# Performance work log

Measured on AMD Instinct MI355X. Metric: run time of the kernel, lower is better.

The kernel has to match this reference:

```python
import jax, jax.numpy as jnp
import numpy as np

CONF_THRESH = 0.01
TOP_K = 200
NMS_THRESH = 0.45


def setup_inputs() -> dict:
    key = jax.random.key(0)
    k1, k2, k3, k4, k5 = jax.random.split(key, 5)
    B, N, C = 32, 8732, 21
    return {
        "loc_data": jax.random.normal(k1, (B, N, 4), jnp.float32),
        "conf_data": jax.random.normal(k2, (B, N, C), jnp.float32),
        "pose_data": jax.random.normal(k3, (B, N, 32), jnp.float32),
        "line_data": jax.random.normal(k4, (B, N, 3), jnp.float32),
        "dbox_list": jax.random.uniform(k5, (N, 4), jnp.float32),
    }


def decode(loc, dbox):
    # loc, dbox: [N,4]; variances 0.1 / 0.2 as in the torch decode()
    cxcy = dbox[:, :2] + loc[:, :2] * 0.1 * dbox[:, 2:]
    wh = dbox[:, 2:] * jnp.exp(loc[:, 2:] * 0.2)
    mins = cxcy - wh / 2.0
    maxs = mins + wh
    return jnp.concatenate([mins, maxs], axis=1)  # [N,4] xyxy


def nms_class(boxes, scores, poses, lines):
    """Greedy NMS for one (batch, class). boxes [N,4], scores [N] (softmax probs).
    Matches torch nm_suppression: candidates are the top_k by score above
    conf_thresh; suppress IoU > overlap; at most top_k kept."""
    s0 = jnp.where(scores > CONF_THRESH, scores, -jnp.inf)
    _, cand_idx = jax.lax.top_k(s0, TOP_K)  # descending-score candidate pool
    cb = boxes[cand_idx]                     # [K,4]
    cs = s0[cand_idx]                        # [K], -inf where below threshold
    x1, y1, x2, y2 = cb[:, 0], cb[:, 1], cb[:, 2], cb[:, 3]
    area = (x2 - x1) * (y2 - y1)
    K = TOP_K
    ar = jnp.arange(K)

    def step(s, _):
        i = jnp.argmax(s)
        take = jnp.isfinite(s[i])
        xx1 = jnp.maximum(x1, x1[i])
        yy1 = jnp.maximum(y1, y1[i])
        xx2 = jnp.minimum(x2, x2[i])
        yy2 = jnp.minimum(y2, y2[i])
        inter = jnp.clip(xx2 - xx1, 0.0) * jnp.clip(yy2 - yy1, 0.0)
        union = area - inter + area[i]
        iou = inter / union
        supp = (iou > NMS_THRESH) | (ar == i)
        s_new = jnp.where(take & supp, -jnp.inf, s)
        return s_new, (i, take)

    _, (pos, take) = jax.lax.scan(step, cs, None, length=K)
    gi = cand_idx[pos]  # global box indices of kept detections [K]
    row = jnp.concatenate(
        [scores[gi][:, None], boxes[gi], poses[gi], lines[gi]], axis=1
    )  # [K, 1+4+32+3] = [200, 40]
    return row * take[:, None].astype(row.dtype)


def reference(loc_data, conf_data, pose_data, line_data, dbox_list):
    conf = jax.nn.softmax(conf_data, axis=-1)                       # [B,N,C]
    boxes = jax.vmap(decode, in_axes=(0, None))(loc_data, dbox_list)  # [B,N,4]
    per_cls = jax.vmap(nms_class, in_axes=(None, 1, None, None))    # over classes
    per_batch = jax.vmap(per_cls, in_axes=(0, 0, 0, 0))             # over batch
    out = per_batch(boxes, conf, pose_data, line_data)              # [B,C,200,40]
    return out.at[:, 0].set(0.0)  # class 0 (background) is skipped in torch loop
```

## Files before the change

kernel.cpp:

```cpp
#include <hip/hip_runtime.h>
#include <math.h>

#define BB 32
#define NN 8732
#define CC 21
#define TOPK 200
#define NPOSE 32
#define NLINE 3
#define NBINS 2048
#define CAP 1024
#define ROWW 40

__device__ __forceinline__ double fexp12(double x) {
  const double LOG2E = 1.4426950408889634074;
  const double LN2HI = 6.93147180369123816490e-01;
  const double LN2LO = 1.90821492927058770002e-10;
  double kd = rint(x * LOG2E);
  double r = fma(-kd, LN2HI, x);
  r = fma(-kd, LN2LO, r);
  double p = 2.08767569878680989792e-09;
  p = fma(p, r, 2.50521083854417187751e-08);
  p = fma(p, r, 2.75573192239858906526e-07);
  p = fma(p, r, 2.75573192239858925110e-06);
  p = fma(p, r, 2.48015873015873015873e-05);
  p = fma(p, r, 1.98412698412698412698e-04);
  p = fma(p, r, 1.38888888888888888889e-03);
  p = fma(p, r, 8.33333333333333333333e-03);
  p = fma(p, r, 4.16666666666666666667e-02);
  p = fma(p, r, 1.66666666666666666667e-01);
  p = fma(p, r, 0.5);
  p = fma(p, r, 1.0);
  p = fma(p, r, 1.0);
  int k = (int)kd;
  k = k < -1020 ? -1020 : (k > 1020 ? 1020 : k);
  double sc = __longlong_as_double((long long)(1023 + k) << 52);
  return p * sc;
}

__device__ __forceinline__ double fexp_t(double x, const double* __restrict__ T) {
  const double INV64 = 1.4426950408889634074 * 64.0;
  const double L64HI = 6.93147180369123816490e-01 / 64.0;
  const double L64LO = 1.90821492927058770002e-10 / 64.0;
  double kd = rint(x * INV64);
  double r = fma(-kd, L64HI, x);
  r = fma(-kd, L64LO, r);
  double p = 4.16666666666666666667e-02;
  p = fma(p, r, 1.66666666666666666667e-01);
  p = fma(p, r, 0.5);
  p = fma(p, r, 1.0);
  p = fma(p, r, 1.0);
  int ki = (int)kd;
  double t = T[ki & 63];
  int e = ki >> 6;
  e = e < -1020 ? -1020 : e;
  double sc = __longlong_as_double((long long)(1023 + e) << 52);
  return (t * p) * sc;
}

__global__ __launch_bounds__(256, 4) void score_kernel(
    const float* __restrict__ conf, float* __restrict__ scores) {
  __shared__ __align__(16) float buf[256 * CC];
  __shared__ double Texp[64];
  const int tid = threadIdx.x;
  const int i0 = blockIdx.x * 256;
  const int base = i0 * CC;
  int total = BB * NN * CC - base;
  if (total > 256 * CC) total = 256 * CC;
  {
    const float4* g4 = (const float4*)(conf + base);
    float4* b4 = (float4*)buf;
    const int n4 = total >> 2;
    for (int t = tid; t < n4; t += 256) b4[t] = g4[t];
  }
  if (tid < 64)
    Texp[tid] = fexp12((double)tid * (6.93147180369123816490e-01 / 64.0));
  __syncthreads();
  const int i = i0 + tid;
  if (i >= BB * NN) return;
  const float* p = buf + tid * CC;
  float x[CC];
#pragma unroll
  for (int c = 0; c < CC; ++c) x[c] = p[c];
  float m = x[0];
#pragma unroll
  for (int c = 1; c < CC; ++c) m = fmaxf(m, x[c]);
  float e[CC];
#pragma unroll
  for (int c = 0; c < CC; ++c) e[c] = (float)fexp_t((double)(x[c] - m), Texp);
  float r0 = e[0] + e[8], r1 = e[1] + e[9], r2 = e[2] + e[10], r3 = e[3] + e[11];
  float r4 = e[4] + e[12], r5 = e[5] + e[13], r6 = e[6] + e[14], r7 = e[7] + e[15];
  float sum = ((r0 + r1) + (r2 + r3)) + ((r4 + r5) + (r6 + r7));
  sum += e[16]; sum += e[17]; sum += e[18]; sum += e[19]; sum += e[20];
  const int b = i / NN, n = i - b * NN;
#pragma unroll
  for (int c = 0; c < CC; ++c)
    scores[((size_t)b * CC + c) * NN + n] = e[c] / sum;
}

__device__ __forceinline__ int score_bin(float s) {
  unsigned u = __float_as_uint(s);
  int bin = (int)(u >> 15) - 30720;
  return bin < 0 ? 0 : (bin > NBINS - 1 ? NBINS - 1 : bin);
}

__device__ __forceinline__ float score_full(const float* conf, int b, int c, int n) {
  const float* p = conf + ((size_t)b * NN + n) * CC;
  float mm = p[0];
  for (int c2 = 1; c2 < CC; ++c2) mm = fmaxf(mm, p[c2]);
  float e[CC];
  for (int c2 = 0; c2 < CC; ++c2) e[c2] = (float)fexp12((double)(p[c2] - mm));
  float r0 = e[0] + e[8], r1 = e[1] + e[9], r2 = e[2] + e[10], r3 = e[3] + e[11];
  float r4 = e[4] + e[12], r5 = e[5] + e[13], r6 = e[6] + e[14], r7 = e[7] + e[15];
  float sum = ((r0 + r1) + (r2 + r3)) + ((r4 + r5) + (r6 + r7));
  sum += e[16]; sum += e[17]; sum += e[18]; sum += e[19]; sum += e[20];
  return e[c] / sum;
}

__global__ __launch_bounds__(256) void nms_kernel(
    const float* __restrict__ loc, const float* __restrict__ conf,
    const float* __restrict__ pose, const float* __restrict__ line,
    const float* __restrict__ dbox, const float* __restrict__ scores,
    int mode, float* __restrict__ out) {
  const int bc = blockIdx.x;
  const int b = bc / CC, c = bc - b * CC;
  const int tid = threadIdx.x;
  const int wv = tid >> 6, lane = tid & 63;
  float* outSlab = out + (size_t)bc * (TOPK * ROWW);
  const float4 z4 = make_float4(0.f, 0.f, 0.f, 0.f);

  if (c == 0) {
    float4* o4 = (float4*)outSlab;
    for (int i = tid; i < TOPK * ROWW / 4; i += 256) o4[i] = z4;
    return;
  }

  __shared__ int hist[NBINS];
  __shared__ __align__(16) unsigned long long ckey[CAP + 16];
  __shared__ float4 cbox[TOPK];
  __shared__ float carea[TOPK];
  __shared__ float sScore[TOPK];
  __shared__ int sIdx[TOPK];
  __shared__ unsigned long long supp[TOPK * 4];
  __shared__ unsigned long long rowAnyBits[4];
  __shared__ int kept[TOPK];
  __shared__ int waveTot[4];
  __shared__ int sBT, sCnt, sKept;

  for (int i = tid; i < NBINS; i += 256) hist[i] = 0;
  if (tid == 0) { sCnt = 0; sBT = 0; }
  __syncthreads();

  const float* scoresB = scores + ((size_t)b * CC + c) * NN;

  float4 v[9];
  if (mode == 1) {
#pragma unroll
    for (int k = 0; k < 8; ++k)
      v[k] = *(const float4*)(scoresB + k * 1024 + tid * 4);
    if (tid < 135)
      v[8] = *(const float4*)(scoresB + 8192 + tid * 4);
    else
      v[8] = make_float4(-1.f, -1.f, -1.f, -1.f);
  } else {
#pragma unroll 1
    for (int k = 0; k < 9; ++k) {
      const int n0 = k * 1024 + (tid << 2);
      if (k < 8 || tid < 135) {
        v[k].x = score_full(conf, b, c, n0 + 0);
        v[k].y = score_full(conf, b, c, n0 + 1);
        v[k].z = score_full(conf, b, c, n0 + 2);
        v[k].w = score_full(conf, b, c, n0 + 3);
      } else {
        v[k] = make_float4(-1.f, -1.f, -1.f, -1.f);
      }
    }
  }

#pragma unroll
  for (int k = 0; k < 9; ++k) {
    if (v[k].x > 0.01f) atomicAdd(&hist[score_bin(v[k].x)], 1);
    if (v[k].y > 0.01f) atomicAdd(&hist[score_bin(v[k].y)], 1);
    if (v[k].z > 0.01f) atomicAdd(&hist[score_bin(v[k].z)], 1);
    if (v[k].w > 0.01f) atomicAdd(&hist[score_bin(v[k].w)], 1);
  }
  __syncthreads();

  int s8 = 0;
#pragma unroll
  for (int k = 0; k < 8; ++k) s8 += hist[tid * 8 + k];
  int cs = s8;
#pragma unroll
  for (int d = 1; d < 64; d <<= 1) {
    int t = __shfl_down(cs, d, 64);
    if (lane + d < 64) cs += t;
  }
  if (lane == 0) waveTot[wv] = cs;
  __syncthreads();
  {
    int higher = 0;
    for (int g = wv + 1; g < 4; ++g) higher += waveTot[g];
    int incl = cs + higher;
    int excl = incl - s8;
    if (excl < TOPK && incl >= TOPK) {
      int cum = excl, bt = tid * 8;
      for (int bin = tid * 8 + 7;; --bin) {
        cum += hist[bin];
        if (cum >= TOPK || bin == tid * 8) { bt = bin; break; }
      }
      sBT = bt;
    }
  }
  __syncthreads();
  const int bt = sBT;

#pragma unroll
  for (int k = 0; k < 9; ++k) {
    float sv[4] = {v[k].x, v[k].y, v[k].z, v[k].w};
#pragma unroll
    for (int j = 0; j < 4; ++j) {
      float s = sv[j];
      if (s > 0.01f && score_bin(s) >= bt) {
        int p = atomicAdd(&sCnt, 1);
        if (p < CAP) {
          unsigned n = (unsigned)(k * 1024 + (tid << 2) + j);
          ckey[p] = ((unsigned long long)__float_as_uint(s) << 32) |
                    (unsigned long long)(0xFFFFFFFFu - n);
        }
      }
    }
  }
  __syncthreads();
  const int M = sCnt < CAP ? sCnt : CAP;
  if (M == 0) {
    float4* o4 = (float4*)outSlab;
    for (int i = tid; i < TOPK * ROWW / 4; i += 256) o4[i] = z4;
    return;
  }
  const int K = M < TOPK ? M : TOPK;
  const int Mpad = (M + 15) & ~15;
  for (int i = M + tid; i < Mpad; i += 256) ckey[i] = 0ull;
  __syncthreads();

  for (int t = tid; t < M; t += 256) {
    unsigned long long kt = ckey[t];
    int r = 0;
    for (int j0 = 0; j0 < Mpad; j0 += 16) {
      ulonglong2 kk[8];
#pragma unroll
      for (int q = 0; q < 8; ++q)
        kk[q] = *(const ulonglong2*)(ckey + j0 + 2 * q);
#pragma unroll
      for (int q = 0; q < 8; ++q) {
        r += (kk[q].x > kt) ? 1 : 0;
        r += (kk[q].y > kt) ? 1 : 0;
      }
    }
    if (r < TOPK) {
      sScore[r] = __uint_as_float((unsigned)(kt >> 32));
      sIdx[r] = (int)(0xFFFFFFFFu - (unsigned)(kt & 0xFFFFFFFFull));
    }
  }
  __syncthreads();

  const float* locB = loc + (size_t)b * NN * 4;
  if (tid < K) {
    int n = sIdx[tid];
    float4 l4 = *(const float4*)(locB + (size_t)n * 4);
    float4 d4 = *(const float4*)(dbox + (size_t)n * 4);
    float cx = d4.x + (l4.x * 0.1f) * d4.z;
    float cy = d4.y + (l4.y * 0.1f) * d4.w;
    float w = d4.z * (float)fexp12((double)(l4.z * 0.2f));
    float h = d4.w * (float)fexp12((double)(l4.w * 0.2f));
    float x1 = cx - w * 0.5f;
    float y1 = cy - h * 0.5f;
    float x2 = x1 + w;
    float y2 = y1 + h;
    cbox[tid] = make_float4(x1, y1, x2, y2);
    carea[tid] = (x2 - x1) * (y2 - y1);
  }
  __syncthreads();

  {
    const double TMID = (double)0.45f + 0x1p-26;
    const int l = wv * 64 + lane;
    const bool lvalid = l < K;
    float4 lb = lvalid ? cbox[l] : z4;
    float lar = lvalid ? carea[l] : 0.f;
    const int jlim = (K < wv * 64 + 63) ? K : (wv * 64 + 63);
    for (int j0 = 0; j0 < jlim; j0 += 8) {
      const int jc = (jlim - j0 < 8) ? (jlim - j0) : 8;
      float4 jb[8];
      float ja[8];
#pragma unroll
      for (int q = 0; q < 8; ++q)
        if (q < jc) { jb[q] = cbox[j0 + q]; ja[q] = carea[j0 + q]; }
      unsigned long long mres[8];
#pragma unroll
      for (int q = 0; q < 8; ++q) {
        if (q < jc) {
          float xx1 = fmaxf(lb.x, jb[q].x);
          float yy1 = fmaxf(lb.y, jb[q].y);
          float xx2 = fminf(lb.z, jb[q].z);
          float yy2 = fminf(lb.w, jb[q].w);
          float iw = fmaxf(xx2 - xx1, 0.0f);
          float ih = fmaxf(yy2 - yy1, 0.0f);
          float inter = iw * ih;
          float uni = (lar - inter) + ja[q];
          double tt = fma(-TMID, (double)uni, (double)inter);
          bool hit = lvalid & (l > (j0 + q)) & (tt > 0.0);
          mres[q] = __ballot((int)hit);
        }
      }
      if (lane == 0) {
#pragma unroll
        for (int q = 0; q < 8; ++q)
          if (q < jc) supp[(j0 + q) * 4 + wv] = mres[q];
      }
    }
    if (lane == 0)
      for (int j = jlim; j < K; ++j) supp[j * 4 + wv] = 0ull;
  }
  __syncthreads();

  {
    bool nz = false;
    if (tid < K)
      nz = (supp[tid * 4 + 0] | supp[tid * 4 + 1] |
            supp[tid * 4 + 2] | supp[tid * 4 + 3]) != 0ull;
    unsigned long long bal = __ballot((int)nz);
    if (lane == 0) rowAnyBits[wv] = bal;
  }
  __syncthreads();

  if (tid == 0) {
    unsigned long long alive[4];
#pragma unroll
    for (int w = 0; w < 4; ++w) {
      int cnt = K - w * 64;
      alive[w] = cnt <= 0 ? 0ull : (cnt >= 64 ? ~0ull : ((1ull << cnt) - 1ull));
    }
    int nk = 0;
#pragma unroll
    for (int w = 0; w < 4; ++w) {
      const unsigned long long raw = rowAnyBits[w];
      while (alive[w]) {
        int bit = __ffsll(alive[w]) - 1;
        int j = w * 64 + bit;
        kept[nk++] = j;
        alive[w] &= ~(1ull << bit);
        if ((raw >> bit) & 1) {
          unsigned long long r0 = supp[j * 4 + 0];
          unsigned long long r1 = supp[j * 4 + 1];
          unsigned long long r2 = supp[j * 4 + 2];
          unsigned long long r3 = supp[j * 4 + 3];
          alive[0] &= ~r0; alive[1] &= ~r1; alive[2] &= ~r2; alive[3] &= ~r3;
        }
      }
    }
    sKept = nk;
  }
  __syncthreads();

  const int nk = sKept;
  const float* poseB = pose + (size_t)b * NN * NPOSE;
  const float* lineB = line + (size_t)b * NN * NLINE;
  for (int t = tid; t < nk; t += 256) {
    int j = kept[t];
    int n = sIdx[j];
    float* row = outSlab + (size_t)t * ROWW;
    float4 bx = cbox[j];
    row[0] = sScore[j];
    row[1] = bx.x;
    row[2] = bx.y;
    row[3] = bx.z;
    row[4] = bx.w;
    const float4* p4 = (const float4*)(poseB + (size_t)n * NPOSE);
#pragma unroll
    for (int q = 0; q < 8; ++q) {
      float4 pv = p4[q];
      row[5 + 4 * q + 0] = pv.x;
      row[5 + 4 * q + 1] = pv.y;
      row[5 + 4 * q + 2] = pv.z;
      row[5 + 4 * q + 3] = pv.w;
    }
    row[37] = lineB[(size_t)n * NLINE + 0];
    row[38] = lineB[(size_t)n * NLINE + 1];
    row[39] = lineB[(size_t)n * NLINE + 2];
  }
  {
    const int zq = (TOPK - nk) * 10;
    float4* o4 = (float4*)(outSlab + (size_t)nk * ROWW);
    for (int q = tid; q < zq; q += 256) o4[q] = z4;
  }
}

extern "C" void kernel_launch(void* const* d_in, const int* in_sizes, int n_in,
                              void* d_out, int out_size, void* d_ws, size_t ws_size,
                              hipStream_t stream) {
  const float* loc  = (const float*)d_in[0];
  const float* conf = (const float*)d_in[1];
  const float* pose = (const float*)d_in[2];
  const float* line = (const float*)d_in[3];
  const float* dbox = (const float*)d_in[4];
  float* out = (float*)d_out;

  const size_t scoreBytes = (size_t)BB * CC * NN * sizeof(float);
  int mode = (ws_size >= scoreBytes) ? 1 : 0;
  float* scores = mode ? (float*)d_ws : nullptr;

  if (mode) {
    const int total = BB * NN;
    score_kernel<<<(total + 255) / 256, 256, 0, stream>>>(conf, scores);
  }
  nms_kernel<<<BB * CC, 256, 0, stream>>>(loc, conf, pose, line, dbox,
                                          scores, mode, out);
}
```

Before: 192.0 us.

## Double NMS block size to 512 threads and split IoU matrix across wave halves

Launches the per-(batch,class) NMS kernel with 512 threads instead of 256. Score loading, histogram prefix scan, rank sort and output writes are re-strided for 512 threads. The pairwise IoU suppression matrix is split so that two waves share each 64-row band, each taking half the column range. The aim is to cut per-block latency in the serial-ish phases, at the cost of a larger block that may lower occupancy and leave threads idle in the single-thread greedy pass.

```diff
diff --git a/kernel.cpp b/kernel.cpp
--- a/kernel.cpp
+++ b/kernel.cpp
@@ -10,6 +10,7 @@
 #define NBINS 2048
 #define CAP 1024
 #define ROWW 40
+#define NT 512
 
 __device__ __forceinline__ double fexp12(double x) {
   const double LOG2E = 1.4426950408889634074;
@@ -116,7 +117,7 @@
   return e[c] / sum;
 }
 
-__global__ __launch_bounds__(256) void nms_kernel(
+__global__ __launch_bounds__(NT, 4) void nms_kernel(
     const float* __restrict__ loc, const float* __restrict__ conf,
     const float* __restrict__ pose, const float* __restrict__ line,
     const float* __restrict__ dbox, const float* __restrict__ scores,
@@ -130,7 +131,7 @@
 
   if (c == 0) {
     float4* o4 = (float4*)outSlab;
-    for (int i = tid; i < TOPK * ROWW / 4; i += 256) o4[i] = z4;
+    for (int i = tid; i < TOPK * ROWW / 4; i += NT) o4[i] = z4;
     return;
   }
 
@@ -143,29 +144,29 @@
   __shared__ unsigned long long supp[TOPK * 4];
   __shared__ unsigned long long rowAnyBits[4];
   __shared__ int kept[TOPK];
-  __shared__ int waveTot[4];
+  __shared__ int waveTot[8];
   __shared__ int sBT, sCnt, sKept;
 
-  for (int i = tid; i < NBINS; i += 256) hist[i] = 0;
+  for (int i = tid; i < NBINS; i += NT) hist[i] = 0;
   if (tid == 0) { sCnt = 0; sBT = 0; }
   __syncthreads();
 
   const float* scoresB = scores + ((size_t)b * CC + c) * NN;
 
-  float4 v[9];
+  float4 v[5];
   if (mode == 1) {
 #pragma unroll
-    for (int k = 0; k < 8; ++k)
-      v[k] = *(const float4*)(scoresB + k * 1024 + tid * 4);
+    for (int k = 0; k < 4; ++k)
+      v[k] = *(const float4*)(scoresB + k * 2048 + tid * 4);
     if (tid < 135)
-      v[8] = *(const float4*)(scoresB + 8192 + tid * 4);
+      v[4] = *(const float4*)(scoresB + 8192 + tid * 4);
     else
-      v[8] = make_float4(-1.f, -1.f, -1.f, -1.f);
+      v[4] = make_float4(-1.f, -1.f, -1.f, -1.f);
   } else {
 #pragma unroll 1
-    for (int k = 0; k < 9; ++k) {
-      const int n0 = k * 1024 + (tid << 2);
-      if (k < 8 || tid < 135) {
+    for (int k = 0; k < 5; ++k) {
+      const int n0 = (k < 4 ? k * 2048 : 8192) + (tid << 2);
+      if (k < 4 || tid < 135) {
         v[k].x = score_full(conf, b, c, n0 + 0);
         v[k].y = score_full(conf, b, c, n0 + 1);
         v[k].z = score_full(conf, b, c, n0 + 2);
@@ -177,7 +178,7 @@
   }
 
 #pragma unroll
-  for (int k = 0; k < 9; ++k) {
+  for (int k = 0; k < 5; ++k) {
     if (v[k].x > 0.01f) atomicAdd(&hist[score_bin(v[k].x)], 1);
     if (v[k].y > 0.01f) atomicAdd(&hist[score_bin(v[k].y)], 1);
     if (v[k].z > 0.01f) atomicAdd(&hist[score_bin(v[k].z)], 1);
@@ -185,10 +186,8 @@
   }
   __syncthreads();
 
-  int s8 = 0;
-#pragma unroll
-  for (int k = 0; k < 8; ++k) s8 += hist[tid * 8 + k];
-  int cs = s8;
+  int s4 = hist[tid * 4] + hist[tid * 4 + 1] + hist[tid * 4 + 2] + hist[tid * 4 + 3];
+  int cs = s4;
 #pragma unroll
   for (int d = 1; d < 64; d <<= 1) {
     int t = __shfl_down(cs, d, 64);
@@ -198,14 +197,14 @@
   __syncthreads();
   {
     int higher = 0;
-    for (int g = wv + 1; g < 4; ++g) higher += waveTot[g];
+    for (int g = wv + 1; g < 8; ++g) higher += waveTot[g];
     int incl = cs + higher;
-    int excl = incl - s8;
+    int excl = incl - s4;
     if (excl < TOPK && incl >= TOPK) {
-      int cum = excl, bt = tid * 8;
-      for (int bin = tid * 8 + 7;; --bin) {
+      int cum = excl, bt = tid * 4;
+      for (int bin = tid * 4 + 3;; --bin) {
         cum += hist[bin];
-        if (cum >= TOPK || bin == tid * 8) { bt = bin; break; }
+        if (cum >= TOPK || bin == tid * 4) { bt = bin; break; }
       }
       sBT = bt;
     }
@@ -214,7 +213,7 @@
   const int bt = sBT;
 
 #pragma unroll
-  for (int k = 0; k < 9; ++k) {
+  for (int k = 0; k < 5; ++k) {
     float sv[4] = {v[k].x, v[k].y, v[k].z, v[k].w};
 #pragma unroll
     for (int j = 0; j < 4; ++j) {
@@ -222,7 +221,7 @@
       if (s > 0.01f && score_bin(s) >= bt) {
         int p = atomicAdd(&sCnt, 1);
         if (p < CAP) {
-          unsigned n = (unsigned)(k * 1024 + (tid << 2) + j);
+          unsigned n = (unsigned)((k < 4 ? k * 2048 : 8192) + (tid << 2) + j);
           ckey[p] = ((unsigned long long)__float_as_uint(s) << 32) |
                     (unsigned long long)(0xFFFFFFFFu - n);
         }
@@ -233,24 +232,24 @@
   const int M = sCnt < CAP ? sCnt : CAP;
   if (M == 0) {
     float4* o4 = (float4*)outSlab;
-    for (int i = tid; i < TOPK * ROWW / 4; i += 256) o4[i] = z4;
+    for (int i = tid; i < TOPK * ROWW / 4; i += NT) o4[i] = z4;
     return;
   }
   const int K = M < TOPK ? M : TOPK;
   const int Mpad = (M + 15) & ~15;
-  for (int i = M + tid; i < Mpad; i += 256) ckey[i] = 0ull;
-  __syncthreads();
-
-  for (int t = tid; t < M; t += 256) {
+  for (int i = M + tid; i < Mpad; i += NT) ckey[i] = 0ull;
+  __syncthreads();
+
+  for (int t = tid; t < M; t += NT) {
     unsigned long long kt = ckey[t];
     int r = 0;
-    for (int j0 = 0; j0 < Mpad; j0 += 16) {
-      ulonglong2 kk[8];
-#pragma unroll
-      for (int q = 0; q < 8; ++q)
+    for (int j0 = 0; j0 < Mpad; j0 += 8) {
+      ulonglong2 kk[4];
+#pragma unroll
+      for (int q = 0; q < 4; ++q)
         kk[q] = *(const ulonglong2*)(ckey + j0 + 2 * q);
 #pragma unroll
-      for (int q = 0; q < 8; ++q) {
+      for (int q = 0; q < 4; ++q) {
         r += (kk[q].x > kt) ? 1 : 0;
         r += (kk[q].y > kt) ? 1 : 0;
       }
@@ -282,21 +281,25 @@
 
   {
     const double TMID = (double)0.45f + 0x1p-26;
-    const int l = wv * 64 + lane;
+    const int lw = wv & 3, half = wv >> 2;
+    const int l = lw * 64 + lane;
     const bool lvalid = l < K;
     float4 lb = lvalid ? cbox[l] : z4;
     float lar = lvalid ? carea[l] : 0.f;
-    const int jlim = (K < wv * 64 + 63) ? K : (wv * 64 + 63);
-    for (int j0 = 0; j0 < jlim; j0 += 8) {
-      const int jc = (jlim - j0 < 8) ? (jlim - j0) : 8;
-      float4 jb[8];
-      float ja[8];
-#pragma unroll
-      for (int q = 0; q < 8; ++q)
+    const int jlim = (K < lw * 64 + 63) ? K : (lw * 64 + 63);
+    const int jmid = jlim >> 1;
+    const int jstart = half ? jmid : 0;
+    const int jend = half ? jlim : jmid;
+    for (int j0 = jstart; j0 < jend; j0 += 4) {
+      const int jc = (jend - j0 < 4) ? (jend - j0) : 4;
+      float4 jb[4];
+      float ja[4];
+#pragma unroll
+      for (int q = 0; q < 4; ++q)
         if (q < jc) { jb[q] = cbox[j0 + q]; ja[q] = carea[j0 + q]; }
-      unsigned long long mres[8];
-#pragma unroll
-      for (int q = 0; q < 8; ++q) {
+      unsigned long long mres[4];
+#pragma unroll
+      for (int q = 0; q < 4; ++q) {
         if (q < jc) {
           float xx1 = fmaxf(lb.x, jb[q].x);
           float yy1 = fmaxf(lb.y, jb[q].y);
@@ -313,16 +316,16 @@
       }
       if (lane == 0) {
 #pragma unroll
-        for (int q = 0; q < 8; ++q)
-          if (q < jc) supp[(j0 + q) * 4 + wv] = mres[q];
-      }
-    }
-    if (lane == 0)
-      for (int j = jlim; j < K; ++j) supp[j * 4 + wv] = 0ull;
-  }
-  __syncthreads();
-
-  {
+        for (int q = 0; q < 4; ++q)
+          if (q < jc) supp[(j0 + q) * 4 + lw] = mres[q];
+      }
+    }
+    if (half == 1 && lane == 0)
+      for (int j = jlim; j < K; ++j) supp[j * 4 + lw] = 0ull;
+  }
+  __syncthreads();
+
+  if (tid < 256) {
     bool nz = false;
     if (tid < K)
       nz = (supp[tid * 4 + 0] | supp[tid * 4 + 1] |
@@ -364,7 +367,7 @@
   const int nk = sKept;
   const float* poseB = pose + (size_t)b * NN * NPOSE;
   const float* lineB = line + (size_t)b * NN * NLINE;
-  for (int t = tid; t < nk; t += 256) {
+  for (int t = tid; t < nk; t += NT) {
     int j = kept[t];
     int n = sIdx[j];
     float* row = outSlab + (size_t)t * ROWW;
@@ -390,7 +393,7 @@
   {
     const int zq = (TOPK - nk) * 10;
     float4* o4 = (float4*)(outSlab + (size_t)nk * ROWW);
-    for (int q = tid; q < zq; q += 256) o4[q] = z4;
+    for (int q = tid; q < zq; q += NT) o4[q] = z4;
   }
 }
 
@@ -412,6 +415,6 @@
     const int total = BB * NN;
     score_kernel<<<(total + 255) / 256, 256, 0, stream>>>(conf, scores);
   }
-  nms_kernel<<<BB * CC, 256, 0, stream>>>(loc, conf, pose, line, dbox,
-                                          scores, mode, out);
-}
+  nms_kernel<<<BB * CC, NT, 0, stream>>>(loc, conf, pose, line, dbox,
+                                         scores, mode, out);
+}
```

New measurement: 182.9 us. -4.7%, faster.
